# Optimization experiments

Measured on AMD Instinct MI355X. Metric: run time of the kernel, lower is better.

## Reference

```python
import jax, jax.numpy as jnp
import numpy as np

B, IN, H, A, K = 8192, 2048, 256, 8192, 512

def setup_inputs() -> dict:
    key = jax.random.key(0)
    ks = jax.random.split(key, 8)
    s1, s2, s3 = 1.0/np.sqrt(IN), 1.0/np.sqrt(H), 1.0/np.sqrt(H)
    return {
        "x": jax.random.normal(ks[0], (B, IN), dtype=jnp.float32),
        "possible_moves": jax.random.randint(ks[1], (B, K), 0, A, dtype=jnp.int64),
        "W1": jax.random.uniform(ks[2], (IN, H), jnp.float32, -s1, s1),
        "b1": jax.random.uniform(ks[3], (H,), jnp.float32, -s1, s1),
        "W2": jax.random.uniform(ks[4], (H, H), jnp.float32, -s2, s2),
        "b2": jax.random.uniform(ks[5], (H,), jnp.float32, -s2, s2),
        "W3": jax.random.uniform(ks[6], (H, A), jnp.float32, -s3, s3),
        "b3": jax.random.uniform(ks[7], (A,), jnp.float32, -s3, s3),
    }

def reference(x, possible_moves, W1, b1, W2, b2, W3, b3):
    h = jax.nn.relu(x @ W1 + b1)
    h = jax.nn.relu(h @ W2 + b2)
    q = h @ W3 + b3                      # [B, A]
    # build per-sample legal-move mask via scatter (replaces torch python loop)
    rows = jnp.arange(q.shape[0])[:, None]
    mask = jnp.zeros(q.shape, q.dtype).at[rows, possible_moves].set(1.0)
    filtered = q * mask
    # faithful to torch: any exact-zero entry (illegal OR q==0) becomes -inf
    return jnp.where(filtered == 0, -jnp.inf, filtered)
```

## Files before the change

### kernel.cpp

```cpp
#include <hip/hip_runtime.h>
#include <math.h>
#include <stdint.h>

#define B_DIM   8192
#define IN_DIM  2048
#define H_DIM   256
#define A_DIM   8192
#define K_MOVES 512

#define NEG_SENTINEL (-3.0e38f)

typedef __attribute__((ext_vector_type(8))) short          short8;
typedef __attribute__((ext_vector_type(8))) unsigned short ushort8;
typedef __attribute__((ext_vector_type(4))) unsigned short ushort4v;
typedef __attribute__((ext_vector_type(4))) float          f32x4;

#define MFMA_16x16x32_BF16(a, b, c) \
    __builtin_amdgcn_mfma_f32_16x16x32_bf16((a), (b), (c), 0, 0, 0)

__device__ __forceinline__ unsigned short f2bf(float f) {
    union { float f; unsigned int u; } v; v.f = f;
    unsigned int r = v.u + 0x7fffu + ((v.u >> 16) & 1u);
    return (unsigned short)(r >> 16);
}

__device__ __forceinline__ ushort8 pack8(float4 a, float4 b) {
    ushort8 o;
    o[0] = f2bf(a.x); o[1] = f2bf(a.y); o[2] = f2bf(a.z); o[3] = f2bf(a.w);
    o[4] = f2bf(b.x); o[5] = f2bf(b.y); o[6] = f2bf(b.z); o[7] = f2bf(b.w);
    return o;
}

__global__ __launch_bounds__(256)
void scatter_mask_kernel(const int* __restrict__ pm,
                         unsigned long long* __restrict__ mask) {
    __shared__ unsigned long long lm[A_DIM / 64];
    const int row = blockIdx.x;
    const int tid = threadIdx.x;
    if (tid < 128) lm[tid] = 0ULL;
    __syncthreads();
    const int* p = pm + (size_t)row * K_MOVES;
#pragma unroll
    for (int s = 0; s < K_MOVES / 256; ++s) {
        int mv = p[s * 256 + tid];
        if (mv < 0) mv = 0;
        if (mv >= A_DIM) mv = A_DIM - 1;
        atomicOr(&lm[mv >> 6], 1ULL << (mv & 63));
    }
    __syncthreads();
    if (tid < 128) mask[(size_t)row * 128 + tid] = lm[tid];
}

__global__ __launch_bounds__(256)
void transpose3_kernel(const float* __restrict__ W1, unsigned short* __restrict__ W1t,
                       const float* __restrict__ W2, unsigned short* __restrict__ W2t,
                       const float* __restrict__ W3, unsigned short* __restrict__ W3t) {
    __shared__ unsigned short tile[32][33];
    const int bid = blockIdx.x;
    const float* in; unsigned short* out; int R, C, bx, by;
    if (bid < 512)      { in = W1; out = W1t; R = IN_DIM; C = H_DIM;
                          bx = bid % 8;          by = bid / 8; }
    else if (bid < 576) { in = W2; out = W2t; R = H_DIM;  C = H_DIM;
                          int t = bid - 512; bx = t % 8;   by = t / 8; }
    else                { in = W3; out = W3t; R = H_DIM;  C = A_DIM;
                          int t = bid - 576; bx = t % 256; by = t / 256; }
    const int tx = threadIdx.x, ty = threadIdx.y;
    int x = bx * 32 + tx;
#pragma unroll
    for (int i = 0; i < 32; i += 8) {
        int y = by * 32 + ty + i;
        tile[ty + i][tx] = f2bf(in[(size_t)y * C + x]);
    }
    __syncthreads();
    int ox = by * 32 + tx;
#pragma unroll
    for (int i = 0; i < 32; i += 8) {
        int oy = bx * 32 + ty + i;
        out[(size_t)oy * R + ox] = tile[tx][ty + i];
    }
}

template <typename AT>
__global__ __launch_bounds__(256)
void gemm_small(const AT* __restrict__ A,
                const unsigned short* __restrict__ Bt,
                const float* __restrict__ bias,
                unsigned short* __restrict__ C,
                int M, int N, int K) {
    constexpr bool A_F32 = (sizeof(AT) == 4);
    constexpr int LDA = 72;
    __shared__ __align__(16) unsigned short As[64 * LDA];
    __shared__ __align__(16) unsigned short Bs[64 * LDA];

    const int tid  = threadIdx.x;
    const int wave = tid >> 6, lane = tid & 63;
    const int quad = lane >> 4, tl = lane & 15;
    const int wm = wave >> 1,  wn = wave & 1;
    const int row0 = blockIdx.y * 64, col0 = blockIdx.x * 64;
    const int sr = tid >> 2;
    const int sk = (tid & 3) * 16;

    f32x4 acc[2][2];
#pragma unroll
    for (int i = 0; i < 2; ++i)
#pragma unroll
        for (int j = 0; j < 2; ++j) acc[i][j] = {0.f, 0.f, 0.f, 0.f};

    const AT* Ap             = A  + (size_t)(row0 + sr) * K + sk;
    const unsigned short* Bp = Bt + (size_t)(col0 + sr) * K + sk;

    float4  pa[4];
    ushort8 pa8[2];
    ushort8 pb[2];

    if constexpr (A_F32) {
#pragma unroll
        for (int q = 0; q < 4; ++q) pa[q] = ((const float4*)Ap)[q];
    } else {
        pa8[0] = ((const ushort8*)Ap)[0];
        pa8[1] = ((const ushort8*)Ap)[1];
    }
    pb[0] = ((const ushort8*)Bp)[0];
    pb[1] = ((const ushort8*)Bp)[1];

    const int iters = K >> 6;
    for (int t = 0; t < iters; ++t) {
        if constexpr (A_F32) {
            *(ushort8*)&As[sr * LDA + sk]     = pack8(pa[0], pa[1]);
            *(ushort8*)&As[sr * LDA + sk + 8] = pack8(pa[2], pa[3]);
        } else {
            *(ushort8*)&As[sr * LDA + sk]     = pa8[0];
            *(ushort8*)&As[sr * LDA + sk + 8] = pa8[1];
        }
        *(ushort8*)&Bs[sr * LDA + sk]     = pb[0];
        *(ushort8*)&Bs[sr * LDA + sk + 8] = pb[1];
        __syncthreads();

        if (t + 1 < iters) {
            const AT* ap             = Ap + (t + 1) * 64;
            const unsigned short* bp = Bp + (t + 1) * 64;
            if constexpr (A_F32) {
#pragma unroll
                for (int q = 0; q < 4; ++q) pa[q] = ((const float4*)ap)[q];
            } else {
                pa8[0] = ((const ushort8*)ap)[0];
                pa8[1] = ((const ushort8*)ap)[1];
            }
            pb[0] = ((const ushort8*)bp)[0];
            pb[1] = ((const ushort8*)bp)[1];
        }

#pragma unroll
        for (int ks = 0; ks < 2; ++ks) {
            short8 af[2], bf[2];
#pragma unroll
            for (int i = 0; i < 2; ++i)
                af[i] = *(const short8*)&As[(wm * 32 + i * 16 + tl) * LDA + ks * 32 + quad * 8];
#pragma unroll
            for (int j = 0; j < 2; ++j)
                bf[j] = *(const short8*)&Bs[(wn * 32 + j * 16 + tl) * LDA + ks * 32 + quad * 8];
#pragma unroll
            for (int i = 0; i < 2; ++i)
#pragma unroll
                for (int j = 0; j < 2; ++j)
                    acc[i][j] = MFMA_16x16x32_BF16(bf[j], af[i], acc[i][j]);
        }
        __syncthreads();
    }

    float4 bj4[2];
#pragma unroll
    for (int j = 0; j < 2; ++j)
        bj4[j] = *(const float4*)&bias[col0 + wn * 32 + j * 16 + quad * 4];
#pragma unroll
    for (int i = 0; i < 2; ++i) {
        const int r = row0 + wm * 32 + i * 16 + tl;
#pragma unroll
        for (int j = 0; j < 2; ++j) {
            ushort4v o;
#pragma unroll
            for (int reg = 0; reg < 4; ++reg) {
                float q = acc[i][j][reg] + ((const float*)&bj4[j])[reg];
                o[reg] = f2bf(fmaxf(q, 0.f));
            }
            *(ushort4v*)&C[(size_t)r * N + col0 + wn * 32 + j * 16 + quad * 4] = o;
        }
    }
}

__global__ __launch_bounds__(256)
void gemm_masked(const unsigned short* __restrict__ A,
                 const unsigned short* __restrict__ Bt,
                 const float* __restrict__ bias,
                 float* __restrict__ C,
                 const unsigned long long* __restrict__ mask,
                 int M, int N, int K) {
    __shared__ __align__(16) unsigned short As[128 * 32];
    __shared__ __align__(16) unsigned short Bs[128 * 32];

    const int tid  = threadIdx.x;
    const int wave = tid >> 6, lane = tid & 63;
    const int quad = lane >> 4, tl = lane & 15;
    const int wm = wave >> 1,  wn = wave & 1;
    const int row0 = blockIdx.y * 128, col0 = blockIdx.x * 128;

    f32x4 acc[4][4];
#pragma unroll
    for (int i = 0; i < 4; ++i)
#pragma unroll
        for (int j = 0; j < 4; ++j) acc[i][j] = {0.f, 0.f, 0.f, 0.f};

    for (int k0 = 0; k0 < K; k0 += 32) {
#pragma unroll
        for (int p = 0; p < 2; ++p) {
            const int c = p * 256 + tid;
            const unsigned short* ga =
                A + (size_t)(row0 + (c >> 2)) * K + k0 + (c & 3) * 8;
            __builtin_amdgcn_global_load_lds(
                (const __attribute__((address_space(1))) void*)ga,
                (__attribute__((address_space(3))) void*)&As[(p * 256 + wave * 64) * 8],
                16, 0, 0);
            const unsigned short* gb =
                Bt + (size_t)(col0 + (c >> 2)) * K + k0 + (c & 3) * 8;
            __builtin_amdgcn_global_load_lds(
                (const __attribute__((address_space(1))) void*)gb,
                (__attribute__((address_space(3))) void*)&Bs[(p * 256 + wave * 64) * 8],
                16, 0, 0);
        }
        __syncthreads();

        short8 af[4], bf[4];
#pragma unroll
        for (int i = 0; i < 4; ++i)
            af[i] = *(const short8*)&As[(wm * 64 + i * 16 + tl) * 32 + quad * 8];
#pragma unroll
        for (int j = 0; j < 4; ++j)
            bf[j] = *(const short8*)&Bs[(wn * 64 + j * 16 + tl) * 32 + quad * 8];
#pragma unroll
        for (int i = 0; i < 4; ++i)
#pragma unroll
            for (int j = 0; j < 4; ++j)
                acc[i][j] = MFMA_16x16x32_BF16(bf[j], af[i], acc[i][j]);
        __syncthreads();
    }

    float4 bj4[4];
#pragma unroll
    for (int j = 0; j < 4; ++j)
        bj4[j] = *(const float4*)&bias[col0 + wn * 64 + j * 16 + quad * 4];

#pragma unroll
    for (int i = 0; i < 4; ++i) {
        const int r = row0 + wm * 64 + i * 16 + tl;
        const unsigned long long w = mask[(size_t)r * (N >> 6) + (col0 >> 6) + wn];
#pragma unroll
        for (int j = 0; j < 4; ++j) {
            float q[4];
#pragma unroll
            for (int reg = 0; reg < 4; ++reg) {
                float v = acc[i][j][reg] + ((const float*)&bj4[j])[reg];
                const int bit = j * 16 + quad * 4 + reg;
                bool legal = (w >> bit) & 1ULL;
                bool ok = legal && (v != 0.f) && (fabsf(v) < 1.0e30f);
                q[reg] = ok ? v : NEG_SENTINEL;
            }
            *(float4*)&C[(size_t)r * N + col0 + wn * 64 + j * 16 + quad * 4] =
                make_float4(q[0], q[1], q[2], q[3]);
        }
    }
}

extern "C" void kernel_launch(void* const* d_in, const int* in_sizes, int n_in,
                              void* d_out, int out_size, void* d_ws, size_t ws_size,
                              hipStream_t stream) {
    const float* x  = (const float*)d_in[0];
    const int*   pm = (const int*)d_in[1];
    const float* W1 = (const float*)d_in[2];
    const float* b1 = (const float*)d_in[3];
    const float* W2 = (const float*)d_in[4];
    const float* b2 = (const float*)d_in[5];
    const float* W3 = (const float*)d_in[6];
    const float* b3 = (const float*)d_in[7];
    float* out = (float*)d_out;

    char* ws = (char*)d_ws;
    unsigned long long* mask = (unsigned long long*)ws;
    unsigned short* W1t = (unsigned short*)(ws + (8ull  << 20));
    unsigned short* W2t = (unsigned short*)(ws + (9ull  << 20));
    unsigned short* W3t = (unsigned short*)(ws + (10ull << 20));
    unsigned short* h1b = (unsigned short*)(ws + (16ull << 20));
    unsigned short* h2b = (unsigned short*)(ws + (20ull << 20));

    transpose3_kernel<<<2624, dim3(32, 8), 0, stream>>>(W1, W1t, W2, W2t, W3, W3t);

    scatter_mask_kernel<<<B_DIM, 256, 0, stream>>>(pm, mask);

    gemm_small<float><<<dim3(H_DIM / 64, B_DIM / 64), 256, 0, stream>>>(
        x, W1t, b1, h1b, B_DIM, H_DIM, IN_DIM);

    gemm_small<unsigned short><<<dim3(H_DIM / 64, B_DIM / 64), 256, 0, stream>>>(
        h1b, W2t, b2, h2b, B_DIM, H_DIM, H_DIM);

    gemm_masked<<<dim3(A_DIM / 128, B_DIM / 128), 256, 0, stream>>>(
        h2b, W3t, b3, out, mask, B_DIM, A_DIM, H_DIM);
}
```

Baseline: 432.7 us.

## Restructure final masked GEMM to stage full-K weight tile once

Replaces the K-looped 128x128 masked GEMM with a 256x128 tile per 512-thread block. The whole 128x256 slice of W3t (64 KB) is loaded into LDS once, and each wave keeps its A rows for the full K in registers, read directly from global memory. This removes the per-k-step barriers and LDS staging of A. The bias is folded into the accumulator initialisation, and masks are prefetched before the single sync. The cost is higher register pressure from holding af[2][8] and bf[8], plus large LDS use, which may limit occupancy.

New measurement: 434.9 us. Within noise of the previous version (+0.5%).

```diff
diff --git a/kernel.cpp b/kernel.cpp
--- a/kernel.cpp
+++ b/kernel.cpp
@@ -188,83 +188,78 @@
     }
 }
 
-__global__ __launch_bounds__(256)
-void gemm_masked(const unsigned short* __restrict__ A,
-                 const unsigned short* __restrict__ Bt,
-                 const float* __restrict__ bias,
-                 float* __restrict__ C,
-                 const unsigned long long* __restrict__ mask,
-                 int M, int N, int K) {
-    __shared__ __align__(16) unsigned short As[128 * 32];
-    __shared__ __align__(16) unsigned short Bs[128 * 32];
+__global__ __launch_bounds__(512)
+void gemm3_once(const unsigned short* __restrict__ A,
+                const unsigned short* __restrict__ Bt,
+                const float* __restrict__ bias,
+                float* __restrict__ C,
+                const unsigned long long* __restrict__ mask) {
+    constexpr int K = H_DIM;
+    constexpr int N = A_DIM;
+    __shared__ __align__(16) unsigned short Bs[8 * 128 * 32];
 
     const int tid  = threadIdx.x;
     const int wave = tid >> 6, lane = tid & 63;
     const int quad = lane >> 4, tl = lane & 15;
-    const int wm = wave >> 1,  wn = wave & 1;
-    const int row0 = blockIdx.y * 128, col0 = blockIdx.x * 128;
-
-    f32x4 acc[4][4];
-#pragma unroll
-    for (int i = 0; i < 4; ++i)
-#pragma unroll
-        for (int j = 0; j < 4; ++j) acc[i][j] = {0.f, 0.f, 0.f, 0.f};
-
-    for (int k0 = 0; k0 < K; k0 += 32) {
-#pragma unroll
-        for (int p = 0; p < 2; ++p) {
-            const int c = p * 256 + tid;
-            const unsigned short* ga =
-                A + (size_t)(row0 + (c >> 2)) * K + k0 + (c & 3) * 8;
-            __builtin_amdgcn_global_load_lds(
-                (const __attribute__((address_space(1))) void*)ga,
-                (__attribute__((address_space(3))) void*)&As[(p * 256 + wave * 64) * 8],
-                16, 0, 0);
-            const unsigned short* gb =
-                Bt + (size_t)(col0 + (c >> 2)) * K + k0 + (c & 3) * 8;
-            __builtin_amdgcn_global_load_lds(
-                (const __attribute__((address_space(1))) void*)gb,
-                (__attribute__((address_space(3))) void*)&Bs[(p * 256 + wave * 64) * 8],
-                16, 0, 0);
-        }
-        __syncthreads();
-
-        short8 af[4], bf[4];
-#pragma unroll
-        for (int i = 0; i < 4; ++i)
-            af[i] = *(const short8*)&As[(wm * 64 + i * 16 + tl) * 32 + quad * 8];
-#pragma unroll
-        for (int j = 0; j < 4; ++j)
-            bf[j] = *(const short8*)&Bs[(wn * 64 + j * 16 + tl) * 32 + quad * 8];
-#pragma unroll
-        for (int i = 0; i < 4; ++i)
-#pragma unroll
-            for (int j = 0; j < 4; ++j)
-                acc[i][j] = MFMA_16x16x32_BF16(bf[j], af[i], acc[i][j]);
-        __syncthreads();
-    }
-
-    float4 bj4[4];
-#pragma unroll
-    for (int j = 0; j < 4; ++j)
-        bj4[j] = *(const float4*)&bias[col0 + wn * 64 + j * 16 + quad * 4];
-
-#pragma unroll
-    for (int i = 0; i < 4; ++i) {
-        const int r = row0 + wm * 64 + i * 16 + tl;
-        const unsigned long long w = mask[(size_t)r * (N >> 6) + (col0 >> 6) + wn];
-#pragma unroll
-        for (int j = 0; j < 4; ++j) {
+    const int row0 = blockIdx.y * 256, col0 = blockIdx.x * 128;
+
+#pragma unroll
+    for (int p = 0; p < 8; ++p) {
+        const int L  = p * 512 + tid;
+        const int c4 = L & 3, n = (L >> 2) & 127, s = L >> 9;
+        const unsigned short* g = Bt + (size_t)(col0 + n) * K + s * 32 + c4 * 8;
+        __builtin_amdgcn_global_load_lds(
+            (const __attribute__((address_space(1))) void*)g,
+            (__attribute__((address_space(3))) void*)&Bs[(p * 512 + wave * 64) * 8],
+            16, 0, 0);
+    }
+
+    const int rw0 = row0 + wave * 32;
+    short8 af[2][8];
+#pragma unroll
+    for (int i = 0; i < 2; ++i)
+#pragma unroll
+        for (int s = 0; s < 8; ++s)
+            af[i][s] = *(const short8*)&A[(size_t)(rw0 + i * 16 + tl) * K + s * 32 + quad * 8];
+
+    unsigned long long mw[2][2];
+#pragma unroll
+    for (int i = 0; i < 2; ++i) {
+        const size_t r = rw0 + i * 16 + tl;
+        mw[i][0] = mask[r * (N >> 6) + (col0 >> 6)];
+        mw[i][1] = mask[r * (N >> 6) + (col0 >> 6) + 1];
+    }
+
+    __syncthreads();
+
+#pragma unroll
+    for (int jj = 0; jj < 8; ++jj) {
+        short8 bf[8];
+#pragma unroll
+        for (int s = 0; s < 8; ++s)
+            bf[s] = *(const short8*)&Bs[((s * 128) + jj * 16 + tl) * 32 + quad * 8];
+
+        const float4 b4 = *(const float4*)&bias[col0 + jj * 16 + quad * 4];
+
+#pragma unroll
+        for (int i = 0; i < 2; ++i) {
+            f32x4 acc = {b4.x, b4.y, b4.z, b4.w};
+#pragma unroll
+            for (int s = 0; s < 8; ++s)
+                acc = MFMA_16x16x32_BF16(bf[s], af[i][s], acc);
+
+            const int r = rw0 + i * 16 + tl;
+            const unsigned long long w = mw[i][jj >> 2];
             float q[4];
 #pragma unroll
             for (int reg = 0; reg < 4; ++reg) {
-                float v = acc[i][j][reg] + ((const float*)&bj4[j])[reg];
-                const int bit = j * 16 + quad * 4 + reg;
+                float v = acc[reg];
+                const int bit = (jj & 3) * 16 + quad * 4 + reg;
                 bool legal = (w >> bit) & 1ULL;
                 bool ok = legal && (v != 0.f) && (fabsf(v) < 1.0e30f);
                 q[reg] = ok ? v : NEG_SENTINEL;
             }
-            *(float4*)&C[(size_t)r * N + col0 + wn * 64 + j * 16 + quad * 4] =
+            *(float4*)&C[(size_t)r * N + col0 + jj * 16 + quad * 4] =
                 make_float4(q[0], q[1], q[2], q[3]);
         }
     }
@@ -301,6 +296,6 @@
     gemm_small<unsigned short><<<dim3(H_DIM / 64, B_DIM / 64), 256, 0, stream>>>(
         h1b, W2t, b2, h2b, B_DIM, H_DIM, H_DIM);
 
-    gemm_masked<<<dim3(A_DIM / 128, B_DIM / 128), 256, 0, stream>>>(
-        h2b, W3t, b3, out, mask, B_DIM, A_DIM, H_DIM);
-}
+    gemm3_once<<<dim3(A_DIM / 128, B_DIM / 256), 512, 0, stream>>>(
+        h2b, W3t, b3, out, mask);
+}
```

## Merge weight-transpose and mask-scatter kernels; shrink layer-1 GEMM row tile to 32

Applied to the files above, without the earlier changes.

Combines the weight transpose/convert kernel and the legal-move bitmask scatter kernel into a single launch, with the block index selecting the role. The first-layer GEMM gets its own kernel with 32-row tiles, which doubles the grid from 512 to 1024 blocks so the K=2048 matmul can spread across more CUs. The aim is less launch overhead and better occupancy for the layer-1 GEMM, at the cost of less reuse of the W1 tile per block.

New measurement: 431.3 us. About the same (-0.3%).

```diff
diff --git a/kernel.cpp b/kernel.cpp
--- a/kernel.cpp
+++ b/kernel.cpp
@@ -32,31 +32,31 @@
 }
 
 __global__ __launch_bounds__(256)
-void scatter_mask_kernel(const int* __restrict__ pm,
-                         unsigned long long* __restrict__ mask) {
-    __shared__ unsigned long long lm[A_DIM / 64];
-    const int row = blockIdx.x;
+void prep_kernel(const float* __restrict__ W1, unsigned short* __restrict__ W1t,
+                 const float* __restrict__ W2, unsigned short* __restrict__ W2t,
+                 const float* __restrict__ W3, unsigned short* __restrict__ W3t,
+                 const int* __restrict__ pm,
+                 unsigned long long* __restrict__ mask) {
+    const int bid = blockIdx.x;
     const int tid = threadIdx.x;
-    if (tid < 128) lm[tid] = 0ULL;
-    __syncthreads();
-    const int* p = pm + (size_t)row * K_MOVES;
-#pragma unroll
-    for (int s = 0; s < K_MOVES / 256; ++s) {
-        int mv = p[s * 256 + tid];
-        if (mv < 0) mv = 0;
-        if (mv >= A_DIM) mv = A_DIM - 1;
-        atomicOr(&lm[mv >> 6], 1ULL << (mv & 63));
-    }
-    __syncthreads();
-    if (tid < 128) mask[(size_t)row * 128 + tid] = lm[tid];
-}
-
-__global__ __launch_bounds__(256)
-void transpose3_kernel(const float* __restrict__ W1, unsigned short* __restrict__ W1t,
-                       const float* __restrict__ W2, unsigned short* __restrict__ W2t,
-                       const float* __restrict__ W3, unsigned short* __restrict__ W3t) {
+    if (bid >= 2624) {
+        __shared__ unsigned long long lm[A_DIM / 64];
+        const int row = bid - 2624;
+        if (tid < 128) lm[tid] = 0ULL;
+        __syncthreads();
+        const int* p = pm + (size_t)row * K_MOVES;
+#pragma unroll
+        for (int s = 0; s < K_MOVES / 256; ++s) {
+            int mv = p[s * 256 + tid];
+            if (mv < 0) mv = 0;
+            if (mv >= A_DIM) mv = A_DIM - 1;
+            atomicOr(&lm[mv >> 6], 1ULL << (mv & 63));
+        }
+        __syncthreads();
+        if (tid < 128) mask[(size_t)row * 128 + tid] = lm[tid];
+        return;
+    }
     __shared__ unsigned short tile[32][33];
-    const int bid = blockIdx.x;
     const float* in; unsigned short* out; int R, C, bx, by;
     if (bid < 512)      { in = W1; out = W1t; R = IN_DIM; C = H_DIM;
                           bx = bid % 8;          by = bid / 8; }
@@ -64,7 +64,7 @@
                           int t = bid - 512; bx = t % 8;   by = t / 8; }
     else                { in = W3; out = W3t; R = H_DIM;  C = A_DIM;
                           int t = bid - 576; bx = t % 256; by = t / 256; }
-    const int tx = threadIdx.x, ty = threadIdx.y;
+    const int tx = tid & 31, ty = tid >> 5;
     int x = bx * 32 + tx;
 #pragma unroll
     for (int i = 0; i < 32; i += 8) {
@@ -80,15 +80,84 @@
     }
 }
 
-template <typename AT>
 __global__ __launch_bounds__(256)
-void gemm_small(const AT* __restrict__ A,
-                const unsigned short* __restrict__ Bt,
-                const float* __restrict__ bias,
-                unsigned short* __restrict__ C,
-                int M, int N, int K) {
-    constexpr bool A_F32 = (sizeof(AT) == 4);
-    constexpr int LDA = 72;
+void gemm1_kernel(const float* __restrict__ A,
+                  const unsigned short* __restrict__ Bt,
+                  const float* __restrict__ bias,
+                  unsigned short* __restrict__ C) {
+    constexpr int K = IN_DIM, N = H_DIM, LDA = 72;
+    __shared__ __align__(16) unsigned short As[32 * LDA];
+    __shared__ __align__(16) unsigned short Bs[64 * LDA];
+
+    const int tid  = threadIdx.x;
+    const int wave = tid >> 6, lane = tid & 63;
+    const int quad = lane >> 4, tl = lane & 15;
+    const int wm = wave >> 1,  wn = wave & 1;
+    const int row0 = blockIdx.y * 32, col0 = blockIdx.x * 64;
+
+    const int sra = tid >> 3, ska = (tid & 7) * 8;
+    const int srb = tid >> 2, skb = (tid & 3) * 16;
+
+    f32x4 acc[2];
+    acc[0] = {0.f, 0.f, 0.f, 0.f};
+    acc[1] = {0.f, 0.f, 0.f, 0.f};
+
+    const float* Ap          = A  + (size_t)(row0 + sra) * K + ska;
+    const unsigned short* Bp = Bt + (size_t)(col0 + srb) * K + skb;
+
+    float4  pa[2];
+    ushort8 pb[2];
+    pa[0] = ((const float4*)Ap)[0];
+    pa[1] = ((const float4*)Ap)[1];
+    pb[0] = ((const ushort8*)Bp)[0];
+    pb[1] = ((const ushort8*)Bp)[1];
+
+    constexpr int iters = K / 64;
+    for (int t = 0; t < iters; ++t) {
+        *(ushort8*)&As[sra * LDA + ska] = pack8(pa[0], pa[1]);
+        *(ushort8*)&Bs[srb * LDA + skb]     = pb[0];
+        *(ushort8*)&Bs[srb * LDA + skb + 8] = pb[1];
+        __syncthreads();
+
+        if (t + 1 < iters) {
+            const float* ap          = Ap + (t + 1) * 64;
+            const unsigned short* bp = Bp + (t + 1) * 64;
+            pa[0] = ((const float4*)ap)[0];
+            pa[1] = ((const float4*)ap)[1];
+            pb[0] = ((const ushort8*)bp)[0];
+            pb[1] = ((const ushort8*)bp)[1];
+        }
+
+#pragma unroll
+        for (int ks = 0; ks < 2; ++ks) {
+            short8 af = *(const short8*)&As[(wm * 16 + tl) * LDA + ks * 32 + quad * 8];
+#pragma unroll
+            for (int j = 0; j < 2; ++j) {
+                short8 bf = *(const short8*)&Bs[(wn * 32 + j * 16 + tl) * LDA + ks * 32 + quad * 8];
+                acc[j] = MFMA_16x16x32_BF16(bf, af, acc[j]);
+            }
+        }
+        __syncthreads();
+    }
+
+    const int r = row0 + wm * 16 + tl;
+#pragma unroll
+    for (int j = 0; j < 2; ++j) {
+        const float4 b4 = *(const float4*)&bias[col0 + wn * 32 + j * 16 + quad * 4];
+        ushort4v o;
+#pragma unroll
+        for (int reg = 0; reg < 4; ++reg)
+            o[reg] = f2bf(fmaxf(acc[j][reg] + ((const float*)&b4)[reg], 0.f));
+        *(ushort4v*)&C[(size_t)r * N + col0 + wn * 32 + j * 16 + quad * 4] = o;
+    }
+}
+
+__global__ __launch_bounds__(256)
+void gemm2_kernel(const unsigned short* __restrict__ A,
+                  const unsigned short* __restrict__ Bt,
+                  const float* __restrict__ bias,
+                  unsigned short* __restrict__ C) {
+    constexpr int K = H_DIM, N = H_DIM, LDA = 72;
     __shared__ __align__(16) unsigned short As[64 * LDA];
     __shared__ __align__(16) unsigned short Bs[64 * LDA];
 
@@ -97,8 +166,7 @@
     const int quad = lane >> 4, tl = lane & 15;
     const int wm = wave >> 1,  wn = wave & 1;
     const int row0 = blockIdx.y * 64, col0 = blockIdx.x * 64;
-    const int sr = tid >> 2;
-    const int sk = (tid & 3) * 16;
+    const int sr = tid >> 2, sk = (tid & 3) * 16;
 
     f32x4 acc[2][2];
 #pragma unroll
@@ -106,48 +174,30 @@
 #pragma unroll
         for (int j = 0; j < 2; ++j) acc[i][j] = {0.f, 0.f, 0.f, 0.f};
 
-    const AT* Ap             = A  + (size_t)(row0 + sr) * K + sk;
+    const unsigned short* Ap = A  + (size_t)(row0 + sr) * K + sk;
     const unsigned short* Bp = Bt + (size_t)(col0 + sr) * K + sk;
 
-    float4  pa[4];
-    ushort8 pa8[2];
-    ushort8 pb[2];
-
-    if constexpr (A_F32) {
-#pragma unroll
-        for (int q = 0; q < 4; ++q) pa[q] = ((const float4*)Ap)[q];
-    } else {
-        pa8[0] = ((const ushort8*)Ap)[0];
-        pa8[1] = ((const ushort8*)Ap)[1];
-    }
-    pb[0] = ((const ushort8*)Bp)[0];
-    pb[1] = ((const ushort8*)Bp)[1];
-
-    const int iters = K >> 6;
+    ushort8 pa8[2], pb[2];
+    pa8[0] = ((const ushort8*)Ap)[0];
+    pa8[1] = ((const ushort8*)Ap)[1];
+    pb[0]  = ((const ushort8*)Bp)[0];
+    pb[1]  = ((const ushort8*)Bp)[1];
+
+    constexpr int iters = K / 64;
     for (int t = 0; t < iters; ++t) {
-        if constexpr (A_F32) {
-            *(ushort8*)&As[sr * LDA + sk]     = pack8(pa[0], pa[1]);
-            *(ushort8*)&As[sr * LDA + sk + 8] = pack8(pa[2], pa[3]);
-        } else {
-            *(ushort8*)&As[sr * LDA + sk]     = pa8[0];
-            *(ushort8*)&As[sr * LDA + sk + 8] = pa8[1];
-        }
+        *(ushort8*)&As[sr * LDA + sk]     = pa8[0];
+        *(ushort8*)&As[sr * LDA + sk + 8] = pa8[1];
         *(ushort8*)&Bs[sr * LDA + sk]     = pb[0];
         *(ushort8*)&Bs[sr * LDA + sk + 8] = pb[1];
         __syncthreads();
 
         if (t + 1 < iters) {
-            const AT* ap             = Ap + (t + 1) * 64;
+            const unsigned short* ap = Ap + (t + 1) * 64;
             const unsigned short* bp = Bp + (t + 1) * 64;
-            if constexpr (A_F32) {
-#pragma unroll
-                for (int q = 0; q < 4; ++q) pa[q] = ((const float4*)ap)[q];
-            } else {
-                pa8[0] = ((const ushort8*)ap)[0];
-                pa8[1] = ((const ushort8*)ap)[1];
-            }
-            pb[0] = ((const ushort8*)bp)[0];
-            pb[1] = ((const ushort8*)bp)[1];
+            pa8[0] = ((const ushort8*)ap)[0];
+            pa8[1] = ((const ushort8*)ap)[1];
+            pb[0]  = ((const ushort8*)bp)[0];
+            pb[1]  = ((const ushort8*)bp)[1];
         }
 
 #pragma unroll
@@ -179,10 +229,8 @@
         for (int j = 0; j < 2; ++j) {
             ushort4v o;
 #pragma unroll
-            for (int reg = 0; reg < 4; ++reg) {
-                float q = acc[i][j][reg] + ((const float*)&bj4[j])[reg];
-                o[reg] = f2bf(fmaxf(q, 0.f));
-            }
+            for (int reg = 0; reg < 4; ++reg)
+                o[reg] = f2bf(fmaxf(acc[i][j][reg] + ((const float*)&bj4[j])[reg], 0.f));
             *(ushort4v*)&C[(size_t)r * N + col0 + wn * 32 + j * 16 + quad * 4] = o;
         }
     }
@@ -291,15 +339,14 @@
     unsigned short* h1b = (unsigned short*)(ws + (16ull << 20));
     unsigned short* h2b = (unsigned short*)(ws + (20ull << 20));
 
-    transpose3_kernel<<<2624, dim3(32, 8), 0, stream>>>(W1, W1t, W2, W2t, W3, W3t);
-
-    scatter_mask_kernel<<<B_DIM, 256, 0, stream>>>(pm, mask);
-
-    gemm_small<float><<<dim3(H_DIM / 64, B_DIM / 64), 256, 0, stream>>>(
-        x, W1t, b1, h1b, B_DIM, H_DIM, IN_DIM);
-
-    gemm_small<unsigned short><<<dim3(H_DIM / 64, B_DIM / 64), 256, 0, stream>>>(
-        h1b, W2t, b2, h2b, B_DIM, H_DIM, H_DIM);
+    prep_kernel<<<2624 + B_DIM, 256, 0, stream>>>(W1, W1t, W2, W2t, W3, W3t,
+                                                  pm, mask);
+
+    gemm1_kernel<<<dim3(H_DIM / 64, B_DIM / 32), 256, 0, stream>>>(
+        x, W1t, b1, h1b);
+
+    gemm2_kernel<<<dim3(H_DIM / 64, B_DIM / 64), 256, 0, stream>>>(
+        h1b, W2t, b2, h2b);
 
     gemm_masked<<<dim3(A_DIM / 128, B_DIM / 128), 256, 0, stream>>>(
         h2b, W3t, b3, out, mask, B_DIM, A_DIM, H_DIM);
```
